# Optimization experiments

Hardware: AMD Instinct MI355X
Metric: run time of the kernel (lower is better)

## Reference

```python
import jax, jax.numpy as jnp
import numpy as np

B, S, D, H, E = 4, 2048, 1024, 16, 64  # batch, seq, d_model, heads, head_dim


def setup_inputs() -> dict:
    root = jax.random.key(0)
    ks = jax.random.split(root, 12)
    std = 0.02
    inp = {
        'query': jax.random.normal(ks[0], (B, S, D), jnp.float32),
        'key':   jax.random.normal(ks[1], (B, S, D), jnp.float32),
        'value': jax.random.normal(ks[2], (B, S, D), jnp.float32),
        # per-head Dense projection params, stacked over heads
        'Wq': jax.random.normal(ks[3], (H, D, E), jnp.float32) * std,
        'bq': jnp.zeros((H, E), jnp.float32),
        'Wk': jax.random.normal(ks[4], (H, D, E), jnp.float32) * std,
        'bk': jnp.zeros((H, E), jnp.float32),
        'Wv': jax.random.normal(ks[5], (H, D, E), jnp.float32) * std,
        'bv': jnp.zeros((H, E), jnp.float32),
        # output Dense back to d_model
        'Wo': jax.random.normal(ks[6], (H * E, D), jnp.float32) * std,
        'bo': jnp.zeros((D,), jnp.float32),
        # head_selector: nn.initializers.uniform() -> U[0, 0.01)
        'head_selector': jax.random.uniform(ks[7], (H,), jnp.float32) * 0.01,
    }
    return inp


def reference(query, key, value, Wq, bq, Wk, bk, Wv, bv, Wo, bo, head_selector):
    head_weights = jax.nn.softmax(head_selector)  # [H]
    # per-head projections (vectorized over heads)
    q = jnp.einsum('bsd,hde->bhse', query, Wq) + bq[None, :, None, :]
    k = jnp.einsum('btd,hde->bhte', key,   Wk) + bk[None, :, None, :]
    v = jnp.einsum('btd,hde->bhte', value, Wv) + bv[None, :, None, :]
    scale = 1.0 / jnp.sqrt(jnp.asarray(E, q.dtype))
    scores = jnp.einsum('bhse,bhte->bhst', q, k) * scale  # [B,H,S,S]
    probs = jax.nn.softmax(scores, axis=-1)
    ctx = jnp.einsum('bhst,bhte->bhse', probs, v)
    ctx = ctx * head_weights[None, :, None, None]  # learned per-head scalar
    combined = jnp.transpose(ctx, (0, 2, 1, 3)).reshape(query.shape[0], query.shape[1], H * E)
    return combined @ Wo + bo
```

## Files before the change

### kernel.cpp

```cpp
#include <hip/hip_runtime.h>


typedef __attribute__((ext_vector_type(8))) short     s16x8;
typedef __attribute__((ext_vector_type(4))) float     f32x4;
typedef __attribute__((ext_vector_type(8))) unsigned short u16x8;
typedef __attribute__((ext_vector_type(4))) unsigned short u16x4;
typedef __attribute__((ext_vector_type(4))) unsigned int   u32x4;

#define GLD16(g, l) __builtin_amdgcn_global_load_lds(                         \
    (const __attribute__((address_space(1))) void*)(g),                       \
    (__attribute__((address_space(3))) void*)(l), 16, 0, 0)

__device__ __forceinline__ unsigned short f2bf(float f) {
  unsigned u = __builtin_bit_cast(unsigned, f);
  u += 0x7fffu + ((u >> 16) & 1u);
  return (unsigned short)(u >> 16);
}

__device__ __forceinline__ f32x4 mfma16(s16x8 a, s16x8 b, f32x4 c) {
  return __builtin_amdgcn_mfma_f32_16x16x32_bf16(a, b, c, 0, 0, 0);
}


__global__ __launch_bounds__(256) void cvt_all(
    const float* __restrict__ q, const float* __restrict__ k,
    const float* __restrict__ v, unsigned short* __restrict__ xq,
    unsigned short* __restrict__ xk, unsigned short* __restrict__ xv) {
  const int z = blockIdx.y;
  const float* in = z == 0 ? q : z == 1 ? k : v;
  unsigned short* out = z == 0 ? xq : z == 1 ? xk : xv;
  const int i = blockIdx.x * 256 + threadIdx.x;
  const float4* p = (const float4*)in;
  float4 a = p[(size_t)i * 2], b = p[(size_t)i * 2 + 1];
  u16x8 r = { f2bf(a.x), f2bf(a.y), f2bf(a.z), f2bf(a.w),
              f2bf(b.x), f2bf(b.y), f2bf(b.z), f2bf(b.w) };
  *(u16x8*)(out + (size_t)i * 8) = r;
}

__global__ __launch_bounds__(256) void pack_all(
    const float* __restrict__ Wq, const float* __restrict__ Wk,
    const float* __restrict__ Wv, const float* __restrict__ Wo,
    unsigned short* __restrict__ WQT, unsigned short* __restrict__ WKT,
    unsigned short* __restrict__ WVT, unsigned short* __restrict__ WOT) {
  __shared__ float t[64][65];
  const int z = blockIdx.z, xb = blockIdx.x, kb = blockIdx.y;
  const int tid = threadIdx.x, kr = tid >> 2, q4 = tid & 3;

  const float* srcp;
  size_t srs;
  if (z < 3) {
    const float* W = z == 0 ? Wq : z == 1 ? Wk : Wv;
    srcp = W + (size_t)xb * 65536 + (size_t)kb * 4096;
    srs = 64;
  } else {
    srcp = Wo + (size_t)kb * 65536 + (size_t)xb * 64;
    srs = 1024;
  }
  unsigned short* dstb =
      (z == 0 ? WQT : z == 1 ? WKT : z == 2 ? WVT : WOT) +
      (size_t)xb * 65536 + (size_t)kb * 64;

#pragma unroll
  for (int j4 = 0; j4 < 4; ++j4) {
    float4 v = *(const float4*)(srcp + (size_t)kr * srs + q4 * 16 + j4 * 4);
    t[kr][q4 * 16 + j4 * 4 + 0] = v.x;
    t[kr][q4 * 16 + j4 * 4 + 1] = v.y;
    t[kr][q4 * 16 + j4 * 4 + 2] = v.z;
    t[kr][q4 * 16 + j4 * 4 + 3] = v.w;
  }
  __syncthreads();

  const int er = tid >> 2;
  u16x8 lo, hi;
#pragma unroll
  for (int j = 0; j < 8; ++j) lo[j] = f2bf(t[q4 * 16 + j][er]);
#pragma unroll
  for (int j = 0; j < 8; ++j) hi[j] = f2bf(t[q4 * 16 + 8 + j][er]);
  unsigned short* d = dstb + (size_t)er * 1024 + q4 * 16;
  *(u16x8*)d = lo;
  *(u16x8*)(d + 8) = hi;
}

__global__ __launch_bounds__(256, 2) void gemm_qkv(
    const unsigned short* __restrict__ Xq, const unsigned short* __restrict__ Xk,
    const unsigned short* __restrict__ Xv,
    const unsigned short* __restrict__ Wqt, const unsigned short* __restrict__ Wkt,
    const unsigned short* __restrict__ Wvt,
    const float* __restrict__ bq, const float* __restrict__ bk,
    const float* __restrict__ bv,
    unsigned short* __restrict__ Qp, unsigned short* __restrict__ Kp,
    unsigned short* __restrict__ Vt) {
  const int z = blockIdx.z;
  const unsigned short* A  = z == 0 ? Xq : z == 1 ? Xk : Xv;
  const unsigned short* Bt = z == 0 ? Wqt : z == 1 ? Wkt : Wvt;
  const float* bias = z == 0 ? bq : z == 1 ? bk : bv;

  __shared__ unsigned short sA[128 * 32], sB[128 * 32];
  const int tid = threadIdx.x, w = tid >> 6, l = tid & 63, g = l >> 4, c = l & 15;
  const int m0 = blockIdx.y * 128, n0 = blockIdx.x * 128;
  const int wrow = (w >> 1) * 64, wcol = (w & 1) * 64;
  const int srow = tid >> 2, sslot = tid & 3;

  f32x4 acc[4][4] = {};

  for (int kt = 0; kt < 32; ++kt) {
    const int k0 = kt * 32;
#pragma unroll
    for (int r = 0; r < 2; ++r) {
      const int row = r * 64 + srow, sr = row >> 1;
      const int sch = (((row & 1) << 2) | sslot) ^ (sr & 7);
      const size_t roff = (size_t)(sr * 2 + (sch >> 2)) * 2048 + k0 * 2 + (sch & 3) * 16;
      GLD16((const char*)A  + (size_t)m0 * 2048 + roff, (char*)sA + r * 4096 + w * 1024);
      GLD16((const char*)Bt + (size_t)n0 * 2048 + roff, (char*)sB + r * 4096 + w * 1024);
    }
    __syncthreads();
    s16x8 af[4], bfr[4];
#pragma unroll
    for (int mi = 0; mi < 4; ++mi) {
      const int row = wrow + mi * 16 + c;
      const int ch = (((row & 1) << 2) | g) ^ ((row >> 1) & 7);
      af[mi] = *(const s16x8*)&sA[(row >> 1) * 64 + ch * 8];
    }
#pragma unroll
    for (int ni = 0; ni < 4; ++ni) {
      const int row = wcol + ni * 16 + c;
      const int ch = (((row & 1) << 2) | g) ^ ((row >> 1) & 7);
      bfr[ni] = *(const s16x8*)&sB[(row >> 1) * 64 + ch * 8];
    }
#pragma unroll
    for (int mi = 0; mi < 4; ++mi)
#pragma unroll
      for (int ni = 0; ni < 4; ++ni)
        acc[mi][ni] = mfma16(af[mi], bfr[ni], acc[mi][ni]);
    __syncthreads();
  }

#pragma unroll
  for (int ni = 0; ni < 4; ++ni) {
    const int n = n0 + wcol + ni * 16 + c;
    const float bn = bias[n];
    const int h = n >> 6, e = n & 63;
#pragma unroll
    for (int mi = 0; mi < 4; ++mi) {
      const int m = m0 + wrow + mi * 16 + 4 * g;
      const int b = m >> 11, s = m & 2047;
      if (z == 2) {
        u16x4 o;
#pragma unroll
        for (int i = 0; i < 4; ++i) o[i] = f2bf(acc[mi][ni][i] + bn);
        *(u16x4*)&Vt[(((size_t)(b * 16 + h) * 64 + e) << 11) + s] = o;
      } else {
        unsigned short* dst = (z == 0) ? Qp : Kp;
        const float scale = (z == 0) ? 0.1803368801111244f : 1.0f;
        const size_t base = (((size_t)(b * 16 + h) << 11) + s) << 6;
#pragma unroll
        for (int i = 0; i < 4; ++i)
          dst[base + (size_t)i * 64 + e] = f2bf((acc[mi][ni][i] + bn) * scale);
      }
    }
  }
}

__global__ __launch_bounds__(256, 4) void attn(
    const unsigned short* __restrict__ Qp, const unsigned short* __restrict__ Kp,
    const unsigned short* __restrict__ Vt, const float* __restrict__ hsel,
    unsigned short* __restrict__ Cmb) {
  __shared__ char smem[16384];

  const int tid = threadIdx.x, w = tid >> 6, l = tid & 63, g = l >> 4, c = l & 15;
  const int L  = blockIdx.x;
  const int Lp = (L & 7) * 128 + (L >> 3);
  const int bh = Lp >> 4, qb = Lp & 15;
  const int b = bh >> 4, h = bh & 15;

  float hm = -1e30f, hs = 0.f;
  for (int i = 0; i < 16; ++i) hm = fmaxf(hm, hsel[i]);
  for (int i = 0; i < 16; ++i) hs += __expf(hsel[i] - hm);
  const float hw = __expf(hsel[h] - hm) / hs;

  const size_t qbase = ((size_t)bh * 2048 + qb * 128 + w * 32) * 64;
  s16x8 qf[2][2];
#pragma unroll
  for (int nt = 0; nt < 2; ++nt)
#pragma unroll
    for (int ks = 0; ks < 2; ++ks)
      qf[nt][ks] = *(const s16x8*)(Qp + qbase + (size_t)(nt * 16 + c) * 64 +
                                   ks * 32 + 8 * g);

  f32x4 accc[4][2] = {};
  f32x4 lacc[2] = {};
  const short ob = (short)0x3F80;
  const s16x8 ones = { ob, ob, ob, ob, ob, ob, ob, ob };

  const size_t kbase = (size_t)bh * 2048 * 128;
  const size_t vbase = (size_t)bh * 64 * 4096;
  const int krow = tid >> 3, kslot = tid & 7;
  const size_t kroff = kbase + (size_t)krow * 128 + (size_t)((kslot ^ (krow & 7)) * 16);
  const int vrow = tid >> 2, vslot = tid & 3, vsr = vrow >> 1;
  const int vsch = (((vrow & 1) << 2) | vslot) ^ (vsr & 7);
  const size_t vroff = vbase + (size_t)(vsr * 2 + (vsch >> 2)) * 4096 + (vsch & 3) * 16;

  GLD16((const char*)Kp + kroff, smem + w * 1024);
  GLD16((const char*)Vt + vroff, smem + 4096 + w * 1024);
  __syncthreads();

  for (int it = 0; it < 64; ++it) {
    const int cur = it & 1;
    if (it + 1 < 64) {
      const size_t t0 = (size_t)(it + 1) * 32;
      GLD16((const char*)Kp + kroff + t0 * 128, smem + (cur ^ 1) * 8192 + w * 1024);
      GLD16((const char*)Vt + vroff + t0 * 2,   smem + (cur ^ 1) * 8192 + 4096 + w * 1024);
    }
    const unsigned short* sK = (const unsigned short*)(smem + cur * 8192);
    const unsigned short* sV = (const unsigned short*)(smem + cur * 8192 + 4096);

    f32x4 st[2][2] = {};
#pragma unroll
    for (int ks = 0; ks < 2; ++ks)
#pragma unroll
      for (int mt = 0; mt < 2; ++mt) {
        const int tr = mt * 16 + c;
        s16x8 kf = *(const s16x8*)&sK[tr * 64 + (((4 * ks + g) ^ (tr & 7)) << 3)];
#pragma unroll
        for (int nt = 0; nt < 2; ++nt)
          st[mt][nt] = mfma16(kf, qf[nt][ks], st[mt][nt]);
      }

    s16x8 pf[2];
#pragma unroll
    for (int nt = 0; nt < 2; ++nt) {
#pragma unroll
      for (int mt = 0; mt < 2; ++mt)
#pragma unroll
        for (int i = 0; i < 4; ++i)
          st[mt][nt][i] = __builtin_amdgcn_exp2f(st[mt][nt][i]);

      unsigned a0, a1, b0, b1;
      asm("v_cvt_pk_bf16_f32 %0, %1, %2" : "=v"(a0) : "v"(st[0][nt][0]), "v"(st[0][nt][1]));
      asm("v_cvt_pk_bf16_f32 %0, %1, %2" : "=v"(a1) : "v"(st[0][nt][2]), "v"(st[0][nt][3]));
      asm("v_cvt_pk_bf16_f32 %0, %1, %2" : "=v"(b0) : "v"(st[1][nt][0]), "v"(st[1][nt][1]));
      asm("v_cvt_pk_bf16_f32 %0, %1, %2" : "=v"(b1) : "v"(st[1][nt][2]), "v"(st[1][nt][3]));
      asm("v_permlane32_swap_b32 %0, %1" : "+v"(a0), "+v"(b0));
      asm("v_permlane16_swap_b32 %0, %1" : "+v"(a0), "+v"(b0));
      asm("v_permlane32_swap_b32 %0, %1" : "+v"(a1), "+v"(b1));
      asm("v_permlane16_swap_b32 %0, %1" : "+v"(a1), "+v"(b1));
      u32x4 pd = { a0, a1, b0, b1 };
      pf[nt] = __builtin_bit_cast(s16x8, pd);
      lacc[nt] = mfma16(ones, pf[nt], lacc[nt]);
    }

#pragma unroll
    for (int et = 0; et < 4; ++et) {
      const int er = et * 16 + c;
      const int ch = (((er & 1) << 2) | g) ^ ((er >> 1) & 7);
      s16x8 vf = *(const s16x8*)&sV[(er >> 1) * 64 + ch * 8];
#pragma unroll
      for (int nt = 0; nt < 2; ++nt)
        accc[et][nt] = mfma16(vf, pf[nt], accc[et][nt]);
    }
    __syncthreads();
  }

#pragma unroll
  for (int nt = 0; nt < 2; ++nt) {
    const float sc = hw / lacc[nt][0];
    const int s = qb * 128 + w * 32 + nt * 16 + c;
    unsigned short* dst = Cmb + (((size_t)(b * 2048 + s)) << 10) + h * 64;
#pragma unroll
    for (int et = 0; et < 4; ++et) {
      u16x4 o = { f2bf(accc[et][nt][0] * sc), f2bf(accc[et][nt][1] * sc),
                  f2bf(accc[et][nt][2] * sc), f2bf(accc[et][nt][3] * sc) };
      *(u16x4*)(dst + et * 16 + 4 * g) = o;
    }
  }
}

__global__ __launch_bounds__(256, 2) void gemm_out(
    const unsigned short* __restrict__ A, const unsigned short* __restrict__ Bt,
    const float* __restrict__ bo, float* __restrict__ out) {
  __shared__ unsigned short sA[128 * 32], sB[128 * 32];
  const int tid = threadIdx.x, w = tid >> 6, l = tid & 63, g = l >> 4, c = l & 15;
  const int m0 = blockIdx.y * 128, n0 = blockIdx.x * 128;
  const int wrow = (w >> 1) * 64, wcol = (w & 1) * 64;
  const int srow = tid >> 2, sslot = tid & 3;

  f32x4 acc[4][4] = {};

  for (int kt = 0; kt < 32; ++kt) {
    const int k0 = kt * 32;
#pragma unroll
    for (int r = 0; r < 2; ++r) {
      const int row = r * 64 + srow, sr = row >> 1;
      const int sch = (((row & 1) << 2) | sslot) ^ (sr & 7);
      const size_t roff = (size_t)(sr * 2 + (sch >> 2)) * 2048 + k0 * 2 + (sch & 3) * 16;
      GLD16((const char*)A  + (size_t)m0 * 2048 + roff, (char*)sA + r * 4096 + w * 1024);
      GLD16((const char*)Bt + (size_t)n0 * 2048 + roff, (char*)sB + r * 4096 + w * 1024);
    }
    __syncthreads();
    s16x8 af[4], bfr[4];
#pragma unroll
    for (int mi = 0; mi < 4; ++mi) {
      const int row = wrow + mi * 16 + c;
      const int ch = (((row & 1) << 2) | g) ^ ((row >> 1) & 7);
      af[mi] = *(const s16x8*)&sA[(row >> 1) * 64 + ch * 8];
    }
#pragma unroll
    for (int ni = 0; ni < 4; ++ni) {
      const int row = wcol + ni * 16 + c;
      const int ch = (((row & 1) << 2) | g) ^ ((row >> 1) & 7);
      bfr[ni] = *(const s16x8*)&sB[(row >> 1) * 64 + ch * 8];
    }
#pragma unroll
    for (int mi = 0; mi < 4; ++mi)
#pragma unroll
      for (int ni = 0; ni < 4; ++ni)
        acc[mi][ni] = mfma16(af[mi], bfr[ni], acc[mi][ni]);
    __syncthreads();
  }

#pragma unroll
  for (int ni = 0; ni < 4; ++ni) {
    const int n = n0 + wcol + ni * 16 + c;
    const float bn = bo[n];
#pragma unroll
    for (int mi = 0; mi < 4; ++mi) {
      const int m = m0 + wrow + mi * 16 + 4 * g;
#pragma unroll
      for (int i = 0; i < 4; ++i)
        out[(size_t)(m + i) * 1024 + n] = acc[mi][ni][i] + bn;
    }
  }
}

extern "C" void kernel_launch(void* const* d_in, const int* in_sizes, int n_in,
                              void* d_out, int out_size, void* d_ws, size_t ws_size,
                              hipStream_t stream) {
  const float* query = (const float*)d_in[0];
  const float* key   = (const float*)d_in[1];
  const float* value = (const float*)d_in[2];
  const float* Wq    = (const float*)d_in[3];
  const float* bq    = (const float*)d_in[4];
  const float* Wk    = (const float*)d_in[5];
  const float* bk    = (const float*)d_in[6];
  const float* Wv    = (const float*)d_in[7];
  const float* bv    = (const float*)d_in[8];
  const float* Wo    = (const float*)d_in[9];
  const float* bo    = (const float*)d_in[10];
  const float* hsel  = (const float*)d_in[11];
  float* out = (float*)d_out;

  char* ws = (char*)d_ws;
  const size_t SZX = 16777216;
  const size_t SZW = 2097152;
  unsigned short* XQ  = (unsigned short*)(ws);
  unsigned short* XK  = (unsigned short*)(ws + SZX);
  unsigned short* XV  = (unsigned short*)(ws + 2 * SZX);
  unsigned short* WQT = (unsigned short*)(ws + 3 * SZX);
  unsigned short* WKT = (unsigned short*)(ws + 3 * SZX + SZW);
  unsigned short* WVT = (unsigned short*)(ws + 3 * SZX + 2 * SZW);
  unsigned short* WOT = (unsigned short*)(ws + 3 * SZX + 3 * SZW);
  unsigned short* QP  = (unsigned short*)(ws + 3 * SZX + 4 * SZW);
  unsigned short* KP  = (unsigned short*)(ws + 4 * SZX + 4 * SZW);
  unsigned short* VTP = (unsigned short*)(ws + 5 * SZX + 4 * SZW);
  unsigned short* CMB = (unsigned short*)(ws + 6 * SZX + 4 * SZW);

  cvt_all<<<dim3(4096, 3), 256, 0, stream>>>(query, key, value, XQ, XK, XV);
  pack_all<<<dim3(16, 16, 4), 256, 0, stream>>>(Wq, Wk, Wv, Wo, WQT, WKT, WVT, WOT);
  gemm_qkv<<<dim3(8, 64, 3), 256, 0, stream>>>(XQ, XK, XV, WQT, WKT, WVT,
                                               bq, bk, bv, QP, KP, VTP);
  attn<<<1024, 256, 0, stream>>>(QP, KP, VTP, hsel, CMB);
  gemm_out<<<dim3(8, 64), 256, 0, stream>>>(CMB, WOT, bo, out);
}
```

Measured before the change: 355.9 us.

## Double-buffer LDS in projection GEMMs and remap blocks across XCDs

Both GEMM kernels now keep two LDS buffers and issue the global-to-LDS loads for the next k-tile before running the MFMAs on the current one, so memory latency can overlap with compute. Block indices are also flattened to 1D and remapped so that consecutive launched blocks, which are spread across the 8 XCDs, land on contiguous tile groups within each XCD, aiming for better L2 reuse. The cost is double the LDS per block, which may limit occupancy, plus a little extra index arithmetic.

Result: faster. 340.6 us (-4.3%).

```diff
diff --git a/kernel.cpp b/kernel.cpp
--- a/kernel.cpp
+++ b/kernel.cpp
@@ -81,6 +81,21 @@
   *(u16x8*)(d + 8) = hi;
 }
 
+#define STAGE_G(BUF, KT)                                                      \
+  {                                                                           \
+    const int k0q = (KT) * 32;                                                \
+    _Pragma("unroll") for (int r = 0; r < 2; ++r) {                           \
+      const int row = r * 64 + srow, sr = row >> 1;                           \
+      const int sch = (((row & 1) << 2) | sslot) ^ (sr & 7);                  \
+      const size_t roff =                                                     \
+          (size_t)(sr * 2 + (sch >> 2)) * 2048 + k0q * 2 + (sch & 3) * 16;    \
+      GLD16((const char*)A + (size_t)m0 * 2048 + roff,                        \
+            (char*)sA[BUF] + r * 4096 + w * 1024);                            \
+      GLD16((const char*)Bt + (size_t)n0 * 2048 + roff,                       \
+            (char*)sB[BUF] + r * 4096 + w * 1024);                            \
+    }                                                                         \
+  }
+
 __global__ __launch_bounds__(256, 2) void gemm_qkv(
     const unsigned short* __restrict__ Xq, const unsigned short* __restrict__ Xk,
     const unsigned short* __restrict__ Xv,
@@ -90,42 +105,40 @@
     const float* __restrict__ bv,
     unsigned short* __restrict__ Qp, unsigned short* __restrict__ Kp,
     unsigned short* __restrict__ Vt) {
-  const int z = blockIdx.z;
+  const int L = blockIdx.x;
+  const int W = (L & 7) * 192 + (L >> 3);
+  const int z = W >> 9, vy = (W >> 3) & 63, vx = W & 7;
+
   const unsigned short* A  = z == 0 ? Xq : z == 1 ? Xk : Xv;
   const unsigned short* Bt = z == 0 ? Wqt : z == 1 ? Wkt : Wvt;
   const float* bias = z == 0 ? bq : z == 1 ? bk : bv;
 
-  __shared__ unsigned short sA[128 * 32], sB[128 * 32];
+  __shared__ unsigned short sA[2][128 * 32], sB[2][128 * 32];
   const int tid = threadIdx.x, w = tid >> 6, l = tid & 63, g = l >> 4, c = l & 15;
-  const int m0 = blockIdx.y * 128, n0 = blockIdx.x * 128;
+  const int m0 = vy * 128, n0 = vx * 128;
   const int wrow = (w >> 1) * 64, wcol = (w & 1) * 64;
   const int srow = tid >> 2, sslot = tid & 3;
 
   f32x4 acc[4][4] = {};
 
+  STAGE_G(0, 0);
+  __syncthreads();
+
   for (int kt = 0; kt < 32; ++kt) {
-    const int k0 = kt * 32;
-#pragma unroll
-    for (int r = 0; r < 2; ++r) {
-      const int row = r * 64 + srow, sr = row >> 1;
-      const int sch = (((row & 1) << 2) | sslot) ^ (sr & 7);
-      const size_t roff = (size_t)(sr * 2 + (sch >> 2)) * 2048 + k0 * 2 + (sch & 3) * 16;
-      GLD16((const char*)A  + (size_t)m0 * 2048 + roff, (char*)sA + r * 4096 + w * 1024);
-      GLD16((const char*)Bt + (size_t)n0 * 2048 + roff, (char*)sB + r * 4096 + w * 1024);
-    }
-    __syncthreads();
+    const int cur = kt & 1;
+    if (kt + 1 < 32) STAGE_G(cur ^ 1, kt + 1);
     s16x8 af[4], bfr[4];
 #pragma unroll
     for (int mi = 0; mi < 4; ++mi) {
       const int row = wrow + mi * 16 + c;
       const int ch = (((row & 1) << 2) | g) ^ ((row >> 1) & 7);
-      af[mi] = *(const s16x8*)&sA[(row >> 1) * 64 + ch * 8];
+      af[mi] = *(const s16x8*)&sA[cur][(row >> 1) * 64 + ch * 8];
     }
 #pragma unroll
     for (int ni = 0; ni < 4; ++ni) {
       const int row = wcol + ni * 16 + c;
       const int ch = (((row & 1) << 2) | g) ^ ((row >> 1) & 7);
-      bfr[ni] = *(const s16x8*)&sB[(row >> 1) * 64 + ch * 8];
+      bfr[ni] = *(const s16x8*)&sB[cur][(row >> 1) * 64 + ch * 8];
     }
 #pragma unroll
     for (int mi = 0; mi < 4; ++mi)
@@ -278,37 +291,36 @@
 __global__ __launch_bounds__(256, 2) void gemm_out(
     const unsigned short* __restrict__ A, const unsigned short* __restrict__ Bt,
     const float* __restrict__ bo, float* __restrict__ out) {
-  __shared__ unsigned short sA[128 * 32], sB[128 * 32];
+  const int L = blockIdx.x;
+  const int W = (L & 7) * 64 + (L >> 3);
+  const int vy = W >> 3, vx = W & 7;
+
+  __shared__ unsigned short sA[2][128 * 32], sB[2][128 * 32];
   const int tid = threadIdx.x, w = tid >> 6, l = tid & 63, g = l >> 4, c = l & 15;
-  const int m0 = blockIdx.y * 128, n0 = blockIdx.x * 128;
+  const int m0 = vy * 128, n0 = vx * 128;
   const int wrow = (w >> 1) * 64, wcol = (w & 1) * 64;
   const int srow = tid >> 2, sslot = tid & 3;
 
   f32x4 acc[4][4] = {};
 
+  STAGE_G(0, 0);
+  __syncthreads();
+
   for (int kt = 0; kt < 32; ++kt) {
-    const int k0 = kt * 32;
-#pragma unroll
-    for (int r = 0; r < 2; ++r) {
-      const int row = r * 64 + srow, sr = row >> 1;
-      const int sch = (((row & 1) << 2) | sslot) ^ (sr & 7);
-      const size_t roff = (size_t)(sr * 2 + (sch >> 2)) * 2048 + k0 * 2 + (sch & 3) * 16;
-      GLD16((const char*)A  + (size_t)m0 * 2048 + roff, (char*)sA + r * 4096 + w * 1024);
-      GLD16((const char*)Bt + (size_t)n0 * 2048 + roff, (char*)sB + r * 4096 + w * 1024);
-    }
-    __syncthreads();
+    const int cur = kt & 1;
+    if (kt + 1 < 32) STAGE_G(cur ^ 1, kt + 1);
     s16x8 af[4], bfr[4];
 #pragma unroll
     for (int mi = 0; mi < 4; ++mi) {
       const int row = wrow + mi * 16 + c;
       const int ch = (((row & 1) << 2) | g) ^ ((row >> 1) & 7);
-      af[mi] = *(const s16x8*)&sA[(row >> 1) * 64 + ch * 8];
+      af[mi] = *(const s16x8*)&sA[cur][(row >> 1) * 64 + ch * 8];
     }
 #pragma unroll
     for (int ni = 0; ni < 4; ++ni) {
       const int row = wcol + ni * 16 + c;
       const int ch = (((row & 1) << 2) | g) ^ ((row >> 1) & 7);
-      bfr[ni] = *(const s16x8*)&sB[(row >> 1) * 64 + ch * 8];
+      bfr[ni] = *(const s16x8*)&sB[cur][(row >> 1) * 64 + ch * 8];
     }
 #pragma unroll
     for (int mi = 0; mi < 4; ++mi)
@@ -366,8 +378,8 @@
 
   cvt_all<<<dim3(4096, 3), 256, 0, stream>>>(query, key, value, XQ, XK, XV);
   pack_all<<<dim3(16, 16, 4), 256, 0, stream>>>(Wq, Wk, Wv, Wo, WQT, WKT, WVT, WOT);
-  gemm_qkv<<<dim3(8, 64, 3), 256, 0, stream>>>(XQ, XK, XV, WQT, WKT, WVT,
-                                               bq, bk, bv, QP, KP, VTP);
+  gemm_qkv<<<1536, 256, 0, stream>>>(XQ, XK, XV, WQT, WKT, WVT,
+                                     bq, bk, bv, QP, KP, VTP);
   attn<<<1024, 256, 0, stream>>>(QP, KP, VTP, hsel, CMB);
-  gemm_out<<<dim3(8, 64), 256, 0, stream>>>(CMB, WOT, bo, out);
-}
+  gemm_out<<<512, 256, 0, stream>>>(CMB, WOT, bo, out);
+}
```
